# Optimization experiments

Measured on AMD Instinct MI355X. Metric: run time of the kernel, lower is better.

Reference implementation:

```python
import jax, jax.numpy as jnp
import numpy as np

MAXGRAD = 2.0


def _forward(im, defgrad, affine):
    B, H, W, C = im.shape
    dt = im.dtype
    c = jnp.asarray(MAXGRAD, dt)
    # logistic growth: c / (1 + (c-1) * exp(-x)), maps defgrad into (0, c)
    dg = c / (1.0 + (c - 1.0) * jnp.exp(-defgrad))
    # integral image -> monotone sampling grid
    x_s = jnp.cumsum(dg[..., 0], axis=2)  # cumulate along width
    y_s = jnp.cumsum(dg[..., 1], axis=1)  # cumulate along height
    grid = jnp.stack([x_s, y_s], axis=-1)  # [B,H,W,2]
    # residual affine: affine + identity, applied in homogeneous coords
    ident = jnp.array([1, 0, 0, 0, 1, 0, 0, 0, 1], dtype=dt)
    A = (affine.reshape(-1, 9) + ident).reshape(B, 3, 3)
    grid3 = jnp.concatenate([grid, jnp.ones((B, H, W, 1), dt)], axis=-1)
    grid3 = jnp.einsum('bhwk,bjk->bhwj', grid3, A)  # matmul(grid, A^T)
    x = grid3[..., 0]
    y = grid3[..., 1]
    # bilinear sampling with clamped corner indices
    x0 = jnp.clip(jnp.floor(x).astype(jnp.int32), 0, W - 1)
    x1 = jnp.clip(jnp.floor(x).astype(jnp.int32) + 1, 0, W - 1)
    y0 = jnp.clip(jnp.floor(y).astype(jnp.int32), 0, H - 1)
    y1 = jnp.clip(jnp.floor(y).astype(jnp.int32) + 1, 0, H - 1)
    bidx = jnp.arange(B, dtype=jnp.int32)[:, None, None]  # batch base index
    Ia = im[bidx, y0, x0]  # [B,H,W,C]
    Ib = im[bidx, y1, x0]
    Ic = im[bidx, y0, x1]
    Id = im[bidx, y1, x1]
    x0f = x0.astype(dt); x1f = x1.astype(dt)
    y0f = y0.astype(dt); y1f = y1.astype(dt)
    wa = ((x1f - x) * (y1f - y))[..., None]
    wb = ((x1f - x) * (y - y0f))[..., None]
    wc = ((x - x0f) * (y1f - y))[..., None]
    wd = ((x - x0f) * (y - y0f))[..., None]
    out = wa * Ia + wb * Ib + wc * Ic + wd * Id
    return out, grid3


def setup_inputs() -> dict:
    key = jax.random.key(0)
    k1, k2, k3 = jax.random.split(key, 3)
    B, H, W, C = 16, 512, 512, 4
    im = jax.random.normal(k1, (B, H, W, C), dtype=jnp.float32)
    defgrad = jax.random.normal(k2, (B, H, W, 2), dtype=jnp.float32)
    affine = jax.random.normal(k3, (B, 9), dtype=jnp.float32) * 0.01
    return {"im": im, "defgrad": defgrad, "affine": affine}


def reference(im, defgrad, affine):
    return _forward(im, defgrad, affine)
```

## Files before the change

kernel.cpp:

```cpp
#include <hip/hip_runtime.h>
#include <math.h>

#define BB 16
#define HH 512
#define WW 512
#define CC 4

__global__ __launch_bounds__(512)
void colscan_kernel(const float2* __restrict__ defgrad, float* __restrict__ ys,
                    int ys_stride) {
    const int wt  = blockIdx.x % (WW / 32);
    const int b   = blockIdx.x / (WW / 32);
    const int col = threadIdx.x & 31;
    const int seg = threadIdx.x >> 5;
    const int SEGH = HH / 16;
    const int w  = wt * 32 + col;
    const int h0 = seg * SEGH;
    const float2* dg = defgrad + (size_t)b * HH * WW;

    float vals[SEGH];
    float s = 0.f;
#pragma unroll
    for (int i = 0; i < SEGH; ++i) {
        float v = dg[(size_t)(h0 + i) * WW + w].y;
        v = 2.0f / (1.0f + expf(-v));
        vals[i] = v;
        s += v;
    }

    __shared__ float part[16][32];
    part[seg][col] = s;
    __syncthreads();

    float run = 0.f;
    for (int j = 0; j < seg; ++j) run += part[j][col];

    const size_t rowbase = ((size_t)b * HH + h0) * WW + w;
#pragma unroll
    for (int i = 0; i < SEGH; ++i) {
        run += vals[i];
        ys[(rowbase + (size_t)i * WW) * (size_t)ys_stride] = run;
    }
}

__global__ __launch_bounds__(512)
void rowscan_sample_kernel(const float4* __restrict__ im4,
                           const float2* __restrict__ defgrad,
                           const float*  __restrict__ affine,
                           const float*  __restrict__ ys, int ys_stride,
                           float4* __restrict__ out4,
                           float*  __restrict__ grid3) {
    const int h = blockIdx.x % HH;
    const int b = blockIdx.x / HH;
    const int w = threadIdx.x;
    const size_t pix = ((size_t)b * HH + h) * WW + w;

    float vx  = defgrad[pix].x;
    float dgx = 2.0f / (1.0f + expf(-vx));

    const int lane = w & 63;
    const int wv   = w >> 6;
    float x = dgx;
#pragma unroll
    for (int off = 1; off < 64; off <<= 1) {
        float n = __shfl_up(x, off, 64);
        if (lane >= off) x += n;
    }
    __shared__ float wsum[8];
    if (lane == 63) wsum[wv] = x;
    __syncthreads();
    float pref = 0.f;
    for (int j = 0; j < wv; ++j) pref += wsum[j];
    const float xs = x + pref;

    const float ysv = ys[pix * (size_t)ys_stride];

    const float* Ab = affine + b * 9;
    const float xg = (Ab[0] + 1.f) * xs + Ab[1] * ysv + Ab[2];
    const float yg = Ab[3] * xs + (Ab[4] + 1.f) * ysv + Ab[5];
    const float wg = Ab[6] * xs + Ab[7] * ysv + (Ab[8] + 1.f);

    const int ix = (int)floorf(xg);
    const int iy = (int)floorf(yg);
    const int x0 = min(max(ix,     0), WW - 1);
    const int x1 = min(max(ix + 1, 0), WW - 1);
    const int y0 = min(max(iy,     0), HH - 1);
    const int y1 = min(max(iy + 1, 0), HH - 1);
    const float x0f = (float)x0, x1f = (float)x1;
    const float y0f = (float)y0, y1f = (float)y1;
    const float wa = (x1f - xg) * (y1f - yg);
    const float wb = (x1f - xg) * (yg - y0f);
    const float wc = (xg - x0f) * (y1f - yg);
    const float wd = (xg - x0f) * (yg - y0f);

    const size_t base = (size_t)b * HH * WW;
    const float4 Ia = im4[base + (size_t)y0 * WW + x0];
    const float4 Ib = im4[base + (size_t)y1 * WW + x0];
    const float4 Ic = im4[base + (size_t)y0 * WW + x1];
    const float4 Id = im4[base + (size_t)y1 * WW + x1];

    float4 o;
    o.x = wa * Ia.x + wb * Ib.x + wc * Ic.x + wd * Id.x;
    o.y = wa * Ia.y + wb * Ib.y + wc * Ic.y + wd * Id.y;
    o.z = wa * Ia.z + wb * Ib.z + wc * Ic.z + wd * Id.z;
    o.w = wa * Ia.w + wb * Ib.w + wc * Ic.w + wd * Id.w;
    out4[pix] = o;

    grid3[pix * 3 + 0] = xg;
    grid3[pix * 3 + 1] = yg;
    grid3[pix * 3 + 2] = wg;
}

extern "C" void kernel_launch(void* const* d_in, const int* in_sizes, int n_in,
                              void* d_out, int out_size, void* d_ws, size_t ws_size,
                              hipStream_t stream) {
    const float* im      = (const float*)d_in[0];
    const float* defgrad = (const float*)d_in[1];
    const float* affine  = (const float*)d_in[2];

    float* out   = (float*)d_out;
    float* grid3 = out + (size_t)BB * HH * WW * CC;

    const size_t ys_bytes = (size_t)BB * HH * WW * sizeof(float);
    float* ys;
    int ys_stride;
    if (ws_size >= ys_bytes) {
        ys = (float*)d_ws;
        ys_stride = 1;
    } else {
        ys = grid3 + 1;
        ys_stride = 3;
    }

    colscan_kernel<<<BB * (WW / 32), 512, 0, stream>>>(
        (const float2*)defgrad, ys, ys_stride);

    rowscan_sample_kernel<<<BB * HH, 512, 0, stream>>>(
        (const float4*)im, (const float2*)defgrad, affine,
        ys, ys_stride, (float4*)out, grid3);
}
```

Measured before the change: 256.7 us.

## Restructure column scan into LDS-staged chunks and batch rows per sample block

The column-scan kernel now narrows each block to 16 columns and walks the height in 128-row chunks staged through LDS. A running carry links the chunks, and each thread holds only a few values, which should cut register pressure and give loads a different coalescing pattern. The sampling kernel now handles 4 rows per block, interleaving the wavefront shuffles for the four scans and loading the affine coefficients once. Its block index is remapped with an XCD-style swizzle for locality. The cost is more syncthreads per column block and fewer, heavier sampling blocks.

```diff
diff --git a/kernel.cpp b/kernel.cpp
--- a/kernel.cpp
+++ b/kernel.cpp
@@ -6,42 +6,75 @@
 #define WW 512
 #define CC 4
 
+#define CS_COLS   16
+#define CS_CHUNK  128
+#define CS_NCHUNK (HH / CS_CHUNK)
+#define CS_SEGS   32
+#define CS_SEGH   (CS_CHUNK / CS_SEGS)
+
 __global__ __launch_bounds__(512)
 void colscan_kernel(const float2* __restrict__ defgrad, float* __restrict__ ys,
                     int ys_stride) {
-    const int wt  = blockIdx.x % (WW / 32);
-    const int b   = blockIdx.x / (WW / 32);
-    const int col = threadIdx.x & 31;
-    const int seg = threadIdx.x >> 5;
-    const int SEGH = HH / 16;
-    const int w  = wt * 32 + col;
-    const int h0 = seg * SEGH;
+    const int wt  = blockIdx.x % (WW / CS_COLS);
+    const int b   = blockIdx.x / (WW / CS_COLS);
+    const int tid = threadIdx.x;
+
+    __shared__ float lds[CS_CHUNK][CS_COLS + 1];
+    __shared__ float part[CS_SEGS][CS_COLS];
+    __shared__ float carry[2][CS_COLS];
+
+    const int lcol = tid & (CS_COLS - 1);
+    const int lrow = tid >> 4;
+    const int scol = tid & (CS_COLS - 1);
+    const int seg  = tid >> 4;
+    const int wcol = wt * CS_COLS + scol;
+
+    if (tid < CS_COLS) carry[0][tid] = 0.f;
+
     const float2* dg = defgrad + (size_t)b * HH * WW;
 
-    float vals[SEGH];
-    float s = 0.f;
-#pragma unroll
-    for (int i = 0; i < SEGH; ++i) {
-        float v = dg[(size_t)(h0 + i) * WW + w].y;
-        v = 2.0f / (1.0f + expf(-v));
-        vals[i] = v;
-        s += v;
-    }
-
-    __shared__ float part[16][32];
-    part[seg][col] = s;
-    __syncthreads();
-
-    float run = 0.f;
-    for (int j = 0; j < seg; ++j) run += part[j][col];
-
-    const size_t rowbase = ((size_t)b * HH + h0) * WW + w;
-#pragma unroll
-    for (int i = 0; i < SEGH; ++i) {
-        run += vals[i];
-        ys[(rowbase + (size_t)i * WW) * (size_t)ys_stride] = run;
+    for (int c = 0; c < CS_NCHUNK; ++c) {
+#pragma unroll
+        for (int k = 0; k < 4; ++k) {
+            const int r = lrow + k * 32;
+            const int grow = c * CS_CHUNK + r;
+            float v = dg[(size_t)grow * WW + wt * CS_COLS + lcol].y;
+            lds[r][lcol] = 2.0f / (1.0f + expf(-v));
+        }
+        __syncthreads();
+
+        float vals[CS_SEGH];
+        float s = 0.f;
+#pragma unroll
+        for (int i = 0; i < CS_SEGH; ++i) {
+            vals[i] = lds[seg * CS_SEGH + i][scol];
+            s += vals[i];
+        }
+        part[seg][scol] = s;
+        const float cold = carry[c & 1][scol];
+        __syncthreads();
+
+        float run = cold, tot = cold;
+#pragma unroll
+        for (int j = 0; j < CS_SEGS; ++j) {
+            float v = part[j][scol];
+            tot += v;
+            if (j < seg) run += v;
+        }
+        if (seg == 0) carry[(c + 1) & 1][scol] = tot;
+
+        const size_t gbase =
+            ((size_t)(b * HH + c * CS_CHUNK + seg * CS_SEGH) * WW + wcol);
+#pragma unroll
+        for (int i = 0; i < CS_SEGH; ++i) {
+            run += vals[i];
+            ys[(gbase + (size_t)i * WW) * (size_t)ys_stride] = run;
+        }
+        __syncthreads();
     }
 }
+
+#define RS_ROWS 4
 
 __global__ __launch_bounds__(512)
 void rowscan_sample_kernel(const float4* __restrict__ im4,
@@ -50,65 +83,92 @@
                            const float*  __restrict__ ys, int ys_stride,
                            float4* __restrict__ out4,
                            float*  __restrict__ grid3) {
-    const int h = blockIdx.x % HH;
-    const int b = blockIdx.x / HH;
-    const int w = threadIdx.x;
-    const size_t pix = ((size_t)b * HH + h) * WW + w;
-
-    float vx  = defgrad[pix].x;
-    float dgx = 2.0f / (1.0f + expf(-vx));
-
+    const int nwg = BB * (HH / RS_ROWS);
+    const int cpx = nwg / 8;
+    const int l   = (blockIdx.x & 7) * cpx + (blockIdx.x >> 3);
+    const int hb  = l % (HH / RS_ROWS);
+    const int b   = l / (HH / RS_ROWS);
+    const int h0  = hb * RS_ROWS;
+
+    const int w    = threadIdx.x;
     const int lane = w & 63;
     const int wv   = w >> 6;
-    float x = dgx;
+
+    const size_t imgbase  = (size_t)b * HH * WW;
+    const size_t rowbase0 = imgbase + (size_t)h0 * WW + w;
+
+    float dgx[RS_ROWS], ysv[RS_ROWS];
+#pragma unroll
+    for (int r = 0; r < RS_ROWS; ++r) {
+        const size_t pix = rowbase0 + (size_t)r * WW;
+        dgx[r] = defgrad[pix].x;
+        ysv[r] = ys[pix * (size_t)ys_stride];
+    }
+#pragma unroll
+    for (int r = 0; r < RS_ROWS; ++r)
+        dgx[r] = 2.0f / (1.0f + expf(-dgx[r]));
+
+    float x0 = dgx[0], x1 = dgx[1], x2 = dgx[2], x3 = dgx[3];
 #pragma unroll
     for (int off = 1; off < 64; off <<= 1) {
-        float n = __shfl_up(x, off, 64);
-        if (lane >= off) x += n;
-    }
-    __shared__ float wsum[8];
-    if (lane == 63) wsum[wv] = x;
+        float n0 = __shfl_up(x0, off, 64);
+        float n1 = __shfl_up(x1, off, 64);
+        float n2 = __shfl_up(x2, off, 64);
+        float n3 = __shfl_up(x3, off, 64);
+        if (lane >= off) { x0 += n0; x1 += n1; x2 += n2; x3 += n3; }
+    }
+    __shared__ float wsum[8][RS_ROWS];
+    if (lane == 63) {
+        wsum[wv][0] = x0; wsum[wv][1] = x1; wsum[wv][2] = x2; wsum[wv][3] = x3;
+    }
     __syncthreads();
-    float pref = 0.f;
-    for (int j = 0; j < wv; ++j) pref += wsum[j];
-    const float xs = x + pref;
-
-    const float ysv = ys[pix * (size_t)ys_stride];
+    float p0 = 0.f, p1 = 0.f, p2 = 0.f, p3 = 0.f;
+    for (int j = 0; j < wv; ++j) {
+        p0 += wsum[j][0]; p1 += wsum[j][1]; p2 += wsum[j][2]; p3 += wsum[j][3];
+    }
+    float xs[RS_ROWS] = { x0 + p0, x1 + p1, x2 + p2, x3 + p3 };
 
     const float* Ab = affine + b * 9;
-    const float xg = (Ab[0] + 1.f) * xs + Ab[1] * ysv + Ab[2];
-    const float yg = Ab[3] * xs + (Ab[4] + 1.f) * ysv + Ab[5];
-    const float wg = Ab[6] * xs + Ab[7] * ysv + (Ab[8] + 1.f);
-
-    const int ix = (int)floorf(xg);
-    const int iy = (int)floorf(yg);
-    const int x0 = min(max(ix,     0), WW - 1);
-    const int x1 = min(max(ix + 1, 0), WW - 1);
-    const int y0 = min(max(iy,     0), HH - 1);
-    const int y1 = min(max(iy + 1, 0), HH - 1);
-    const float x0f = (float)x0, x1f = (float)x1;
-    const float y0f = (float)y0, y1f = (float)y1;
-    const float wa = (x1f - xg) * (y1f - yg);
-    const float wb = (x1f - xg) * (yg - y0f);
-    const float wc = (xg - x0f) * (y1f - yg);
-    const float wd = (xg - x0f) * (yg - y0f);
-
-    const size_t base = (size_t)b * HH * WW;
-    const float4 Ia = im4[base + (size_t)y0 * WW + x0];
-    const float4 Ib = im4[base + (size_t)y1 * WW + x0];
-    const float4 Ic = im4[base + (size_t)y0 * WW + x1];
-    const float4 Id = im4[base + (size_t)y1 * WW + x1];
-
-    float4 o;
-    o.x = wa * Ia.x + wb * Ib.x + wc * Ic.x + wd * Id.x;
-    o.y = wa * Ia.y + wb * Ib.y + wc * Ic.y + wd * Id.y;
-    o.z = wa * Ia.z + wb * Ib.z + wc * Ic.z + wd * Id.z;
-    o.w = wa * Ia.w + wb * Ib.w + wc * Ic.w + wd * Id.w;
-    out4[pix] = o;
-
-    grid3[pix * 3 + 0] = xg;
-    grid3[pix * 3 + 1] = yg;
-    grid3[pix * 3 + 2] = wg;
+    const float a00 = Ab[0] + 1.f, a01 = Ab[1], a02 = Ab[2];
+    const float a10 = Ab[3], a11 = Ab[4] + 1.f, a12 = Ab[5];
+    const float a20 = Ab[6], a21 = Ab[7], a22 = Ab[8] + 1.f;
+
+#pragma unroll
+    for (int r = 0; r < RS_ROWS; ++r) {
+        const size_t pix = rowbase0 + (size_t)r * WW;
+        const float xg = a00 * xs[r] + a01 * ysv[r] + a02;
+        const float yg = a10 * xs[r] + a11 * ysv[r] + a12;
+        const float wg = a20 * xs[r] + a21 * ysv[r] + a22;
+
+        const int ix = (int)floorf(xg);
+        const int iy = (int)floorf(yg);
+        const int cx0 = min(max(ix,     0), WW - 1);
+        const int cx1 = min(max(ix + 1, 0), WW - 1);
+        const int cy0 = min(max(iy,     0), HH - 1);
+        const int cy1 = min(max(iy + 1, 0), HH - 1);
+        const float x0f = (float)cx0, x1f = (float)cx1;
+        const float y0f = (float)cy0, y1f = (float)cy1;
+        const float wa = (x1f - xg) * (y1f - yg);
+        const float wb = (x1f - xg) * (yg - y0f);
+        const float wc = (xg - x0f) * (y1f - yg);
+        const float wd = (xg - x0f) * (yg - y0f);
+
+        const float4 Ia = im4[imgbase + (size_t)cy0 * WW + cx0];
+        const float4 Ib = im4[imgbase + (size_t)cy1 * WW + cx0];
+        const float4 Ic = im4[imgbase + (size_t)cy0 * WW + cx1];
+        const float4 Id = im4[imgbase + (size_t)cy1 * WW + cx1];
+
+        float4 o;
+        o.x = wa * Ia.x + wb * Ib.x + wc * Ic.x + wd * Id.x;
+        o.y = wa * Ia.y + wb * Ib.y + wc * Ic.y + wd * Id.y;
+        o.z = wa * Ia.z + wb * Ib.z + wc * Ic.z + wd * Id.z;
+        o.w = wa * Ia.w + wb * Ib.w + wc * Ic.w + wd * Id.w;
+        out4[pix] = o;
+
+        grid3[pix * 3 + 0] = xg;
+        grid3[pix * 3 + 1] = yg;
+        grid3[pix * 3 + 2] = wg;
+    }
 }
 
 extern "C" void kernel_launch(void* const* d_in, const int* in_sizes, int n_in,
@@ -132,10 +192,10 @@
         ys_stride = 3;
     }
 
-    colscan_kernel<<<BB * (WW / 32), 512, 0, stream>>>(
+    colscan_kernel<<<BB * (WW / CS_COLS), 512, 0, stream>>>(
         (const float2*)defgrad, ys, ys_stride);
 
-    rowscan_sample_kernel<<<BB * HH, 512, 0, stream>>>(
+    rowscan_sample_kernel<<<BB * (HH / RS_ROWS), 512, 0, stream>>>(
         (const float4*)im, (const float2*)defgrad, affine,
         ys, ys_stride, (float4*)out, grid3);
 }
```

Measured after the change: 250.2 us. 2.5% less time.
